# Performance work log

Measured on AMD Instinct MI355X. Metric: run time of the kernel, lower is better.

## Reference

```python
import jax, jax.numpy as jnp
import numpy as np

B, N, H, ITERS = 4, 4096, 128, 8
EPS = 1e-5  # torch LayerNorm default


def _mlp(x, w1, b1, w2, b2, w3, b3):
    x = jax.nn.relu(x @ w1.T + b1)
    x = jax.nn.relu(x @ w2.T + b2)
    return x @ w3.T + b3


def setup_inputs() -> dict:
    key = jax.random.key(0)
    ks = jax.random.split(key, 16)
    s = 0.05
    nrm = lambda k, shape: jax.random.normal(k, shape, jnp.float32) * s
    z = lambda *shape: jnp.zeros(shape, jnp.float32)
    return {
        "x": jax.random.normal(ks[0], (B, N, N), jnp.float32),
        "k": jax.random.uniform(ks[1], (B,), jnp.float32, 1.0, 10.0),
        "n": jax.random.uniform(ks[2], (B,), jnp.float32, 10.0, 100.0),
        "mask": (jax.random.uniform(ks[3], (B, N)) < 0.9).astype(jnp.float32),
        # init MLP: 2 -> H -> H -> H (torch Linear convention: [out, in])
        "init_w1": nrm(ks[4], (H, 2)), "init_b1": z(H),
        "init_w2": nrm(ks[5], (H, H)), "init_b2": z(H),
        "init_w3": nrm(ks[6], (H, H)), "init_b3": z(H),
        # msg MLP: H -> H -> H -> H
        "msg_w1": nrm(ks[7], (H, H)), "msg_b1": z(H),
        "msg_w2": nrm(ks[8], (H, H)), "msg_b2": z(H),
        "msg_w3": nrm(ks[9], (H, H)), "msg_b3": z(H),
        # LSTMCell (gate order i, f, g, o)
        "lstm_wih": nrm(ks[10], (4 * H, H)), "lstm_whh": nrm(ks[11], (4 * H, H)),
        "lstm_bih": z(4 * H), "lstm_bhh": z(4 * H),
        # LayerNorm affine
        "ln_g": jnp.ones(H, jnp.float32), "ln_b": z(H),
        # vote MLP: H -> H -> H -> 1
        "vote_w1": nrm(ks[12], (H, H)), "vote_b1": z(H),
        "vote_w2": nrm(ks[13], (H, H)), "vote_b2": z(H),
        "vote_w3": nrm(ks[14], (1, H)), "vote_b3": z(1),
    }


def reference(x, k, n, mask,
              init_w1, init_b1, init_w2, init_b2, init_w3, init_b3,
              msg_w1, msg_b1, msg_w2, msg_b2, msg_w3, msg_b3,
              lstm_wih, lstm_whh, lstm_bih, lstm_bhh,
              ln_g, ln_b,
              vote_w1, vote_b1, vote_w2, vote_b2, vote_w3, vote_b3):
    b, n_node, _ = x.shape

    def ln(h):
        mu = h.mean(-1, keepdims=True)
        xc = h - mu
        var = (xc * xc).mean(-1, keepdims=True)
        return xc * jax.lax.rsqrt(var + EPS) * ln_g + ln_b

    nk = jnp.stack([k, n], axis=1)                          # [B, 2]
    init0 = _mlp(nk, init_w1, init_b1, init_w2, init_b2, init_w3, init_b3)
    h = jnp.broadcast_to(init0[:, None, :], (b, n_node, init0.shape[-1]))  # [B, N, H]
    c = jnp.zeros_like(h)
    embed = ln(h)
    for _ in range(ITERS):
        m = _mlp(embed, msg_w1, msg_b1, msg_w2, msg_b2, msg_w3, msg_b3)   # [B, N, H]
        msg = jnp.einsum('bij,bjh->bih', x, m)                            # dense aggregation
        gates = msg @ lstm_wih.T + lstm_bih + h @ lstm_whh.T + lstm_bhh   # [B, N, 4H]
        i, f, g, o = jnp.split(gates, 4, axis=-1)
        c = jax.nn.sigmoid(f) * c + jax.nn.sigmoid(i) * jnp.tanh(g)
        h = jax.nn.sigmoid(o) * jnp.tanh(c)
        embed = ln(h)
    vote = _mlp(embed, vote_w1, vote_b1, vote_w2, vote_b2, vote_w3, vote_b3)[..., 0]  # [B, N]
    return jax.nn.sigmoid((vote * mask).sum(axis=1))        # [B]
```

## Files before the change

kernel.cpp:

```cpp
#include <hip/hip_runtime.h>
#include <cstddef>
#include <cstdint>

#define LN_EPS 1e-5f

typedef __attribute__((ext_vector_type(8))) short bf16x8;
typedef __attribute__((ext_vector_type(4))) float f32x4;

__device__ __forceinline__ unsigned short f2bf(float f) {
    unsigned u = __float_as_uint(f);
    u += 0x7FFFu + ((u >> 16) & 1u);
    return (unsigned short)(u >> 16);
}
__device__ __forceinline__ float sigf(float x) { return 1.f / (1.f + __expf(-x)); }

__device__ __forceinline__ void gload_lds16(const void* g, void* l) {
    __builtin_amdgcn_global_load_lds(
        (const __attribute__((address_space(1))) unsigned int*)(unsigned long long)(uintptr_t)g,
        (__attribute__((address_space(3))) unsigned int*)(unsigned int)(uintptr_t)l,
        16, 0, 0);
}

__device__ __forceinline__ void layer128(const unsigned short* __restrict__ W,
                                         const bf16x8 a[4], f32x4 acc[8],
                                         int lr, int lq)
{
#pragma unroll
    for (int s = 0; s < 4; ++s) {
#pragma unroll
        for (int tn = 0; tn < 8; ++tn) {
            bf16x8 b = *(const bf16x8*)(W + (tn * 16 + lr) * 128 + s * 32 + lq * 8);
            acc[tn] = __builtin_amdgcn_mfma_f32_16x16x32_bf16(a[s], b, acc[tn], 0, 0, 0);
        }
    }
}

__global__ __launch_bounds__(256)
void msg_mlp_kernel(const unsigned short* __restrict__ embed,
                    const unsigned short* __restrict__ w1, const float* __restrict__ b1,
                    const unsigned short* __restrict__ w2, const float* __restrict__ b2,
                    const unsigned short* __restrict__ w3, const float* __restrict__ b3,
                    unsigned short* __restrict__ m_t, int N)
{
    __shared__ unsigned short sact[4][16][136];
    const int lane = threadIdx.x & 63, wave = threadIdx.x >> 6;
    const int lr = lane & 15, lq = lane >> 4;
    const int r0 = (blockIdx.x * 4 + wave) * 16;

    bf16x8 a[4];
    f32x4 acc[8];

#pragma unroll
    for (int s = 0; s < 4; ++s)
        a[s] = *(const bf16x8*)(embed + (long long)(r0 + lr) * 128 + s * 32 + lq * 8);
#pragma unroll
    for (int tn = 0; tn < 8; ++tn) acc[tn] = (f32x4)(0.f);
    layer128(w1, a, acc, lr, lq);

#pragma unroll
    for (int tn = 0; tn < 8; ++tn) {
        float bb = b1[tn * 16 + lr];
#pragma unroll
        for (int r = 0; r < 4; ++r) {
            float v = acc[tn][r] + bb; v = v > 0.f ? v : 0.f;
            sact[wave][lq * 4 + r][tn * 16 + lr] = f2bf(v);
        }
    }
    __syncthreads();
#pragma unroll
    for (int s = 0; s < 4; ++s)
        a[s] = *(const bf16x8*)&sact[wave][lr][s * 32 + lq * 8];
#pragma unroll
    for (int tn = 0; tn < 8; ++tn) acc[tn] = (f32x4)(0.f);
    layer128(w2, a, acc, lr, lq);

#pragma unroll
    for (int tn = 0; tn < 8; ++tn) {
        float bb = b2[tn * 16 + lr];
#pragma unroll
        for (int r = 0; r < 4; ++r) {
            float v = acc[tn][r] + bb; v = v > 0.f ? v : 0.f;
            sact[wave][lq * 4 + r][tn * 16 + lr] = f2bf(v);
        }
    }
    __syncthreads();
#pragma unroll
    for (int s = 0; s < 4; ++s)
        a[s] = *(const bf16x8*)&sact[wave][lr][s * 32 + lq * 8];
#pragma unroll
    for (int tn = 0; tn < 8; ++tn) acc[tn] = (f32x4)(0.f);
    layer128(w3, a, acc, lr, lq);

    const int batch = r0 / N;
    const int rin0 = r0 - batch * N + lq * 4;
#pragma unroll
    for (int tn = 0; tn < 8; ++tn) {
        float bb = b3[tn * 16 + lr];
        ushort4 o;
        o.x = f2bf(acc[tn][0] + bb); o.y = f2bf(acc[tn][1] + bb);
        o.z = f2bf(acc[tn][2] + bb); o.w = f2bf(acc[tn][3] + bb);
        *(ushort4*)(m_t + ((long long)(batch * 128 + tn * 16 + lr)) * N + rin0) = o;
    }
}

__global__ __launch_bounds__(256)
void agg_mfma_kernel(const unsigned short* __restrict__ xb,
                     const unsigned short* __restrict__ mt,
                     float* __restrict__ msgp, int N, long long BNH)
{
    __shared__ short sA[128 * 64];
    __shared__ short sB[128 * 64];

    const int tid = threadIdx.x;
    const int lane = tid & 63, w = tid >> 6;
    const int lr = lane & 15, lq = lane >> 4;
    const int wr = w & 1, wc = w >> 1;
    const int r0 = blockIdx.x * 128;
    const int ksp = blockIdx.y;
    const int batch = blockIdx.z;
    const int kbase = ksp * (N >> 2);
    const int nsteps = (N >> 2) >> 6;

    const unsigned short* xrow = xb + (long long)batch * N * N;
    const unsigned short* mrow = mt + (long long)batch * 128 * N;

    f32x4 acc[4][4];
#pragma unroll
    for (int tr = 0; tr < 4; ++tr)
#pragma unroll
        for (int tn = 0; tn < 4; ++tn) acc[tr][tn] = (f32x4)(0.f);

    for (int step = 0; step < nsteps; ++step) {
        const int k0 = kbase + step * 64;
#pragma unroll
        for (int j = 0; j < 4; ++j) {
            const int c = ((w * 4 + j) << 6) + lane;
            const unsigned short* g = xrow + (long long)(r0 + (c >> 3)) * N + k0 + (c & 7) * 8;
            gload_lds16(g, (char*)sA + (w * 4 + j) * 1024);
        }
#pragma unroll
        for (int j = 0; j < 4; ++j) {
            const int c = ((w * 4 + j) << 6) + lane;
            const unsigned short* g = mrow + (long long)(c >> 3) * N + k0 + (c & 7) * 8;
            gload_lds16(g, (char*)sB + (w * 4 + j) * 1024);
        }
        __syncthreads();
#pragma unroll
        for (int ks = 0; ks < 2; ++ks) {
            bf16x8 af[4], bfr[4];
#pragma unroll
            for (int tr = 0; tr < 4; ++tr)
                af[tr] = *(const bf16x8*)((const char*)sA + (wr * 64 + tr * 16 + lr) * 128 + ks * 64 + lq * 16);
#pragma unroll
            for (int tn = 0; tn < 4; ++tn)
                bfr[tn] = *(const bf16x8*)((const char*)sB + (wc * 64 + tn * 16 + lr) * 128 + ks * 64 + lq * 16);
#pragma unroll
            for (int tr = 0; tr < 4; ++tr)
#pragma unroll
                for (int tn = 0; tn < 4; ++tn)
                    acc[tr][tn] = __builtin_amdgcn_mfma_f32_16x16x32_bf16(af[tr], bfr[tn], acc[tr][tn], 0, 0, 0);
        }
        __syncthreads();
    }

    float* outb = msgp + (long long)ksp * BNH + (long long)(batch * N + r0) * 128;
#pragma unroll
    for (int tr = 0; tr < 4; ++tr)
#pragma unroll
        for (int tn = 0; tn < 4; ++tn)
#pragma unroll
            for (int r = 0; r < 4; ++r)
                outb[(long long)(wr * 64 + tr * 16 + lq * 4 + r) * 128 + wc * 64 + tn * 16 + lr] = acc[tr][tn][r];
}

__global__ __launch_bounds__(256)
void agg_fallback_kernel(const float* __restrict__ xf,
                         const unsigned short* __restrict__ mt, float* __restrict__ msgp0,
                         int N)
{
    __shared__ float sacc[4][16][132];
    const int lane = threadIdx.x & 63, wave = threadIdx.x >> 6;
    const int lr = lane & 15, lq = lane >> 4;
    const int batch = blockIdx.y;
    const int rowBase = blockIdx.x * 16;
    const int kBase = wave * (N >> 2);
    const int kIters = N >> 7;

    const float* af = xf + (long long)batch * N * N + (long long)(rowBase + lr) * N + kBase + lq * 8;
    const long long bbase = (long long)batch * 128 * N + (long long)lr * N + kBase + lq * 8;

    f32x4 acc[8];
#pragma unroll
    for (int tn = 0; tn < 8; ++tn) acc[tn] = (f32x4)(0.f);

    for (int it = 0; it < kIters; ++it) {
        const int k = it * 32;
        float4 lo = *(const float4*)(af + k);
        float4 hi = *(const float4*)(af + k + 4);
        bf16x8 a0;
        a0[0] = (short)f2bf(lo.x); a0[1] = (short)f2bf(lo.y);
        a0[2] = (short)f2bf(lo.z); a0[3] = (short)f2bf(lo.w);
        a0[4] = (short)f2bf(hi.x); a0[5] = (short)f2bf(hi.y);
        a0[6] = (short)f2bf(hi.z); a0[7] = (short)f2bf(hi.w);
#pragma unroll
        for (int tn = 0; tn < 8; ++tn) {
            bf16x8 b0 = *(const bf16x8*)(mt + bbase + (long long)tn * 16 * N + k);
            acc[tn] = __builtin_amdgcn_mfma_f32_16x16x32_bf16(a0, b0, acc[tn], 0, 0, 0);
        }
    }

#pragma unroll
    for (int tn = 0; tn < 8; ++tn)
#pragma unroll
        for (int r = 0; r < 4; ++r)
            sacc[wave][lq * 4 + r][tn * 16 + lr] = acc[tn][r];
    __syncthreads();
    {
        const int t = threadIdx.x;
        const int row = t >> 4, cb2 = (t & 15) * 8;
        float o[8];
#pragma unroll
        for (int j = 0; j < 8; ++j)
            o[j] = sacc[0][row][cb2 + j] + sacc[1][row][cb2 + j]
                 + sacc[2][row][cb2 + j] + sacc[3][row][cb2 + j];
        float* dst = msgp0 + (long long)(batch * N + rowBase + row) * 128 + cb2;
        *(float4*)dst = make_float4(o[0], o[1], o[2], o[3]);
        *(float4*)(dst + 4) = make_float4(o[4], o[5], o[6], o[7]);
    }
}

template<int NPART>
__global__ __launch_bounds__(256)
void gates_lstm_kernel(const float* __restrict__ msgp, long long BNH,
                       unsigned short* hb, float* cb,
                       const unsigned short* __restrict__ wih,
                       const unsigned short* __restrict__ whh,
                       const float* __restrict__ bih, const float* __restrict__ bhh,
                       const float* __restrict__ lng, const float* __restrict__ lnb,
                       unsigned short* __restrict__ embed_out)
{
    __shared__ float sred[4][16][2];
    const int lane = threadIdx.x & 63, wave = threadIdx.x >> 6;
    const int lr = lane & 15, lq = lane >> 4;
    const int r0 = blockIdx.x * 16;

    f32x4 acc[8];
#pragma unroll
    for (int t = 0; t < 8; ++t) acc[t] = (f32x4)(0.f);

    bf16x8 a[4];
#pragma unroll
    for (int s = 0; s < 4; ++s) {
        const long long base = (long long)(r0 + lr) * 128 + s * 32 + lq * 8;
        float v[8];
        {
            float4 t0 = *(const float4*)(msgp + base);
            float4 t1 = *(const float4*)(msgp + base + 4);
            v[0] = t0.x; v[1] = t0.y; v[2] = t0.z; v[3] = t0.w;
            v[4] = t1.x; v[5] = t1.y; v[6] = t1.z; v[7] = t1.w;
        }
#pragma unroll
        for (int j = 1; j < NPART; ++j) {
            float4 t0 = *(const float4*)(msgp + j * BNH + base);
            float4 t1 = *(const float4*)(msgp + j * BNH + base + 4);
            v[0] += t0.x; v[1] += t0.y; v[2] += t0.z; v[3] += t0.w;
            v[4] += t1.x; v[5] += t1.y; v[6] += t1.z; v[7] += t1.w;
        }
        bf16x8 r8;
#pragma unroll
        for (int e = 0; e < 8; ++e) r8[e] = (short)f2bf(v[e]);
        a[s] = r8;
    }
#pragma unroll
    for (int s = 0; s < 4; ++s)
#pragma unroll
        for (int tt = 0; tt < 8; ++tt) {
            const int brow = (tt >> 1) * 128 + wave * 32 + (tt & 1) * 16 + lr;
            bf16x8 b = *(const bf16x8*)(wih + brow * 128 + s * 32 + lq * 8);
            acc[tt] = __builtin_amdgcn_mfma_f32_16x16x32_bf16(a[s], b, acc[tt], 0, 0, 0);
        }
#pragma unroll
    for (int s = 0; s < 4; ++s)
        a[s] = *(const bf16x8*)((const unsigned short*)hb + (long long)(r0 + lr) * 128 + s * 32 + lq * 8);
#pragma unroll
    for (int s = 0; s < 4; ++s)
#pragma unroll
        for (int tt = 0; tt < 8; ++tt) {
            const int brow = (tt >> 1) * 128 + wave * 32 + (tt & 1) * 16 + lr;
            bf16x8 b = *(const bf16x8*)(whh + brow * 128 + s * 32 + lq * 8);
            acc[tt] = __builtin_amdgcn_mfma_f32_16x16x32_bf16(a[s], b, acc[tt], 0, 0, 0);
        }

    float hn[2][4];
    float4* cw = (float4*)cb;
#pragma unroll
    for (int half = 0; half < 2; ++half) {
        const int col = wave * 32 + half * 16 + lr;
        const float bi  = bih[col]       + bhh[col];
        const float bf_ = bih[col + 128] + bhh[col + 128];
        const float bg  = bih[col + 256] + bhh[col + 256];
        const float bo  = bih[col + 384] + bhh[col + 384];
        const long long cidx = ((long long)blockIdx.x * 8 + wave * 2 + half) * 64 + lane;
        float4 cold = cw[cidx];
        float co[4] = {cold.x, cold.y, cold.z, cold.w};
        float cn[4];
#pragma unroll
        for (int r = 0; r < 4; ++r) {
            float iv = acc[0 + half][r] + bi;
            float fv = acc[2 + half][r] + bf_;
            float gv = acc[4 + half][r] + bg;
            float ov = acc[6 + half][r] + bo;
            float cc = sigf(fv) * co[r] + sigf(iv) * tanhf(gv);
            cn[r] = cc;
            hn[half][r] = sigf(ov) * tanhf(cc);
        }
        float4 cnew = {cn[0], cn[1], cn[2], cn[3]};
        cw[cidx] = cnew;
    }

    float ps1[4], ps2[4];
#pragma unroll
    for (int r = 0; r < 4; ++r) {
        float s1 = hn[0][r] + hn[1][r];
        float s2 = hn[0][r] * hn[0][r] + hn[1][r] * hn[1][r];
#pragma unroll
        for (int m = 1; m <= 8; m <<= 1) {
            s1 += __shfl_xor(s1, m);
            s2 += __shfl_xor(s2, m);
        }
        ps1[r] = s1; ps2[r] = s2;
    }
    if (lr == 0) {
#pragma unroll
        for (int r = 0; r < 4; ++r) {
            sred[wave][lq * 4 + r][0] = ps1[r];
            sred[wave][lq * 4 + r][1] = ps2[r];
        }
    }
    __syncthreads();

#pragma unroll
    for (int half = 0; half < 2; ++half) {
        const int col = wave * 32 + half * 16 + lr;
        const float g = lng[col], bb = lnb[col];
#pragma unroll
        for (int r = 0; r < 4; ++r) {
            const int row = lq * 4 + r;
            float S1 = sred[0][row][0] + sred[1][row][0] + sred[2][row][0] + sred[3][row][0];
            float S2 = sred[0][row][1] + sred[1][row][1] + sred[2][row][1] + sred[3][row][1];
            float mean = S1 * (1.f / 128.f);
            float var  = S2 * (1.f / 128.f) - mean * mean;
            float rs = rsqrtf(var + LN_EPS);
            long long off = (long long)(r0 + row) * 128 + col;
            hb[off] = f2bf(hn[half][r]);
            embed_out[off] = f2bf((hn[half][r] - mean) * rs * g + bb);
        }
    }
}

__global__ __launch_bounds__(256)
void vote_mlp_kernel(const unsigned short* __restrict__ embed,
                     const unsigned short* __restrict__ w1, const float* __restrict__ b1,
                     const unsigned short* __restrict__ w2, const float* __restrict__ b2,
                     const float* __restrict__ w3, const float* __restrict__ b3p,
                     const float* __restrict__ mask, float* __restrict__ logit, int N)
{
    __shared__ unsigned short sact[4][16][136];
    const int lane = threadIdx.x & 63, wave = threadIdx.x >> 6;
    const int lr = lane & 15, lq = lane >> 4;
    const int r0 = (blockIdx.x * 4 + wave) * 16;

    bf16x8 a[4];
    f32x4 acc[8];
#pragma unroll
    for (int s = 0; s < 4; ++s)
        a[s] = *(const bf16x8*)(embed + (long long)(r0 + lr) * 128 + s * 32 + lq * 8);
#pragma unroll
    for (int tn = 0; tn < 8; ++tn) acc[tn] = (f32x4)(0.f);
    layer128(w1, a, acc, lr, lq);

#pragma unroll
    for (int tn = 0; tn < 8; ++tn) {
        float bb = b1[tn * 16 + lr];
#pragma unroll
        for (int r = 0; r < 4; ++r) {
            float v = acc[tn][r] + bb; v = v > 0.f ? v : 0.f;
            sact[wave][lq * 4 + r][tn * 16 + lr] = f2bf(v);
        }
    }
    __syncthreads();
#pragma unroll
    for (int s = 0; s < 4; ++s)
        a[s] = *(const bf16x8*)&sact[wave][lr][s * 32 + lq * 8];
#pragma unroll
    for (int tn = 0; tn < 8; ++tn) acc[tn] = (f32x4)(0.f);
    layer128(w2, a, acc, lr, lq);

    float dot[4] = {0.f, 0.f, 0.f, 0.f};
#pragma unroll
    for (int tn = 0; tn < 8; ++tn) {
        const int col = tn * 16 + lr;
        const float bb = b2[col], w3c = w3[col];
#pragma unroll
        for (int r = 0; r < 4; ++r) {
            float v = acc[tn][r] + bb; v = v > 0.f ? v : 0.f;
            dot[r] += v * w3c;
        }
    }
#pragma unroll
    for (int r = 0; r < 4; ++r)
#pragma unroll
        for (int m = 1; m <= 8; m <<= 1) dot[r] += __shfl_xor(dot[r], m);

    const int batch = r0 / N;
    const float b3 = b3p[0];
    const int base = r0 + lq * 4;
    float wsum = mask[base + 0] * (dot[0] + b3) + mask[base + 1] * (dot[1] + b3)
               + mask[base + 2] * (dot[2] + b3) + mask[base + 3] * (dot[3] + b3);
    float t = (lr == 0) ? wsum : 0.f;
    t += __shfl_xor(t, 16);
    t += __shfl_xor(t, 32);
    if (lane == 0) atomicAdd(&logit[batch], t);
}

__global__ __launch_bounds__(128)
void init_kernel(const float* __restrict__ kk, const float* __restrict__ nn,
                 const float* __restrict__ w1, const float* __restrict__ b1,
                 const float* __restrict__ w2, const float* __restrict__ b2,
                 const float* __restrict__ w3, const float* __restrict__ b3,
                 const float* __restrict__ lng, const float* __restrict__ lnb,
                 float* __restrict__ init0, float* __restrict__ embed0,
                 float* __restrict__ logit, int H)
{
    int b = blockIdx.x, j = threadIdx.x;
    __shared__ float s1[128];
    __shared__ float s2[128];
    __shared__ float red[128];
    if (j == 0) logit[b] = 0.f;
    float kv = kk[b], nv = nn[b];
    float h1 = w1[j * 2 + 0] * kv + w1[j * 2 + 1] * nv + b1[j];
    h1 = h1 > 0.f ? h1 : 0.f;
    s1[j] = h1; __syncthreads();
    float h2 = b2[j];
    for (int q = 0; q < H; ++q) h2 += w2[j * H + q] * s1[q];
    h2 = h2 > 0.f ? h2 : 0.f;
    s2[j] = h2; __syncthreads();
    float o = b3[j];
    for (int q = 0; q < H; ++q) o += w3[j * H + q] * s2[q];
    init0[b * H + j] = o;

    red[j] = o; __syncthreads();
    for (int s = 64; s > 0; s >>= 1) { if (j < s) red[j] += red[j + s]; __syncthreads(); }
    float mu = red[0] / (float)H;
    __syncthreads();
    float d = o - mu;
    red[j] = d * d; __syncthreads();
    for (int s = 64; s > 0; s >>= 1) { if (j < s) red[j] += red[j + s]; __syncthreads(); }
    float var = red[0] / (float)H;
    embed0[b * H + j] = d * rsqrtf(var + LN_EPS) * lng[j] + lnb[j];
}

__global__ void bcast_kernel(const float* __restrict__ init0, const float* __restrict__ embed0,
                             unsigned short* __restrict__ hb, float* __restrict__ cb,
                             unsigned short* __restrict__ embed,
                             long long total, long long NH)
{
    long long idx = (long long)blockIdx.x * blockDim.x + threadIdx.x;
    if (idx >= total) return;
    int b = (int)(idx / NH);
    int j = (int)(idx & 127);
    hb[idx] = f2bf(init0[b * 128 + j]);
    embed[idx] = f2bf(embed0[b * 128 + j]);
    cb[idx] = 0.f;
}

__global__ void cast_kernel(const float* __restrict__ x, unsigned short* __restrict__ xb,
                            long long n4)
{
    long long i = ((long long)blockIdx.x * blockDim.x + threadIdx.x);
    if (i >= n4) return;
    float4 v = *(const float4*)(x + i * 4);
    ushort4 o;
    o.x = f2bf(v.x); o.y = f2bf(v.y); o.z = f2bf(v.z); o.w = f2bf(v.w);
    *(ushort4*)&xb[i * 4] = o;
}

struct CastArgs {
    const float* src[7];
    unsigned short* dst[7];
    int n[7];
};

__global__ void castw_kernel(CastArgs a)
{
    int rg = blockIdx.y;
    int i = (blockIdx.x * blockDim.x + threadIdx.x) * 4;
    if (i < a.n[rg]) {
        float4 v = *(const float4*)(a.src[rg] + i);
        ushort4 o;
        o.x = f2bf(v.x); o.y = f2bf(v.y); o.z = f2bf(v.z); o.w = f2bf(v.w);
        *(ushort4*)(a.dst[rg] + i) = o;
    }
}

__global__ void sigmoid_kernel(const float* __restrict__ logit, float* __restrict__ out, int B)
{
    int b = threadIdx.x;
    if (b < B) out[b] = 1.f / (1.f + __expf(-logit[b]));
}

extern "C" void kernel_launch(void* const* d_in, const int* in_sizes, int n_in,
                              void* d_out, int out_size, void* d_ws, size_t ws_size,
                              hipStream_t stream)
{
    const float* x    = (const float*)d_in[0];
    const float* kk   = (const float*)d_in[1];
    const float* nn   = (const float*)d_in[2];
    const float* mask = (const float*)d_in[3];
    const float* iw1  = (const float*)d_in[4];
    const float* ib1  = (const float*)d_in[5];
    const float* iw2  = (const float*)d_in[6];
    const float* ib2  = (const float*)d_in[7];
    const float* iw3  = (const float*)d_in[8];
    const float* ib3  = (const float*)d_in[9];
    const float* mw1  = (const float*)d_in[10];
    const float* mb1  = (const float*)d_in[11];
    const float* mw2  = (const float*)d_in[12];
    const float* mb2  = (const float*)d_in[13];
    const float* mw3  = (const float*)d_in[14];
    const float* mb3  = (const float*)d_in[15];
    const float* wih  = (const float*)d_in[16];
    const float* whh  = (const float*)d_in[17];
    const float* bih  = (const float*)d_in[18];
    const float* bhh  = (const float*)d_in[19];
    const float* lng  = (const float*)d_in[20];
    const float* lnb  = (const float*)d_in[21];
    const float* vw1  = (const float*)d_in[22];
    const float* vb1  = (const float*)d_in[23];
    const float* vw2  = (const float*)d_in[24];
    const float* vb2  = (const float*)d_in[25];
    const float* vw3  = (const float*)d_in[26];
    const float* vb3  = (const float*)d_in[27];
    float* out = (float*)d_out;

    const int B = in_sizes[1];
    const int H = in_sizes[5];
    const int N = in_sizes[3] / B;
    const long long NH  = (long long)N * H;
    const long long BNH = (long long)B * NH;
    const int M = B * N;

    char* p = (char*)d_ws;
    auto alloc = [&](long long bytes) {
        char* q = p; p += (bytes + 255) & ~255LL; return q;
    };
    float*          cb     = (float*)alloc(BNH * 4);
    unsigned short* embed  = (unsigned short*)alloc(BNH * 2);
    unsigned short* hb     = (unsigned short*)alloc(BNH * 2);
    unsigned short* m_t    = (unsigned short*)alloc(BNH * 2);
    float*          msgp   = (float*)alloc(4 * BNH * 4);
    float*          init0  = (float*)alloc((long long)B * H * 4);
    float*          embed0 = (float*)alloc((long long)B * H * 4);
    float*          logit  = (float*)alloc((long long)B * 4);
    unsigned short* wb_m1  = (unsigned short*)alloc((long long)H * H * 2);
    unsigned short* wb_m2  = (unsigned short*)alloc((long long)H * H * 2);
    unsigned short* wb_m3  = (unsigned short*)alloc((long long)H * H * 2);
    unsigned short* wb_ih  = (unsigned short*)alloc(4LL * H * H * 2);
    unsigned short* wb_hh  = (unsigned short*)alloc(4LL * H * H * 2);
    unsigned short* wb_v1  = (unsigned short*)alloc((long long)H * H * 2);
    unsigned short* wb_v2  = (unsigned short*)alloc((long long)H * H * 2);
    unsigned short* x_bf   = (unsigned short*)alloc(2LL * B * N * N);
    const bool use_xb = ((long long)(p - (char*)d_ws) <= (long long)ws_size);

    init_kernel<<<B, H, 0, stream>>>(kk, nn, iw1, ib1, iw2, ib2, iw3, ib3, lng, lnb,
                                     init0, embed0, logit, H);
    {
        long long nb = (BNH + 255) / 256;
        bcast_kernel<<<dim3((unsigned)nb), 256, 0, stream>>>(init0, embed0, hb, cb, embed, BNH, NH);
    }
    {
        CastArgs ca;
        ca.src[0] = mw1; ca.dst[0] = wb_m1; ca.n[0] = H * H;
        ca.src[1] = mw2; ca.dst[1] = wb_m2; ca.n[1] = H * H;
        ca.src[2] = mw3; ca.dst[2] = wb_m3; ca.n[2] = H * H;
        ca.src[3] = wih; ca.dst[3] = wb_ih; ca.n[3] = 4 * H * H;
        ca.src[4] = whh; ca.dst[4] = wb_hh; ca.n[4] = 4 * H * H;
        ca.src[5] = vw1; ca.dst[5] = wb_v1; ca.n[5] = H * H;
        ca.src[6] = vw2; ca.dst[6] = wb_v2; ca.n[6] = H * H;
        castw_kernel<<<dim3(64, 7), 256, 0, stream>>>(ca);
    }
    if (use_xb) {
        long long n4 = (long long)B * N * N / 4;
        cast_kernel<<<dim3((unsigned)((n4 + 255) / 256)), 256, 0, stream>>>(x, x_bf, n4);
    }

    dim3 gridRow(M / 64);
    dim3 gridRow16(M / 16);
    dim3 gridAggNew(N / 128, 4, B);
    dim3 gridAggOld(N / 16, B);

    for (int it = 0; it < 8; ++it) {
        msg_mlp_kernel<<<gridRow, 256, 0, stream>>>(embed, wb_m1, mb1, wb_m2, mb2,
                                                    wb_m3, mb3, m_t, N);
        if (use_xb) {
            agg_mfma_kernel<<<gridAggNew, 256, 0, stream>>>(x_bf, m_t, msgp, N, BNH);
            gates_lstm_kernel<4><<<gridRow16, 256, 0, stream>>>(msgp, BNH, hb, cb, wb_ih, wb_hh,
                                                                bih, bhh, lng, lnb, embed);
        } else {
            agg_fallback_kernel<<<gridAggOld, 256, 0, stream>>>(x, m_t, msgp, N);
            gates_lstm_kernel<1><<<gridRow16, 256, 0, stream>>>(msgp, BNH, hb, cb, wb_ih, wb_hh,
                                                                bih, bhh, lng, lnb, embed);
        }
    }

    vote_mlp_kernel<<<gridRow, 256, 0, stream>>>(embed, wb_v1, vb1, wb_v2, vb2,
                                                 vw3, vb3, mask, logit, N);
    sigmoid_kernel<<<1, 64, 0, stream>>>(logit, out, B);
}
```

Baseline: 1.268 ms.

## Switch dense aggregation to FP8 MFMA with double-buffered swizzled LDS

Casts x and the message matrix to FP8 and runs the dense aggregation with the 16x16x32 fp8 MFMA. K-tiles grow to 128 and are double-buffered in LDS, with an XOR swizzle against bank conflicts. Split-K partial sums are stored as bf16 instead of fp32 to halve partial traffic into the LSTM gates kernel. The aim is to halve the bytes read from x per iteration and raise MFMA throughput, at the cost of much lower precision in the aggregation. The fallback path now writes fp32 into a buffer sized for bf16, which looks undersized.

```diff
diff --git a/kernel.cpp b/kernel.cpp
--- a/kernel.cpp
+++ b/kernel.cpp
@@ -11,6 +11,9 @@
     unsigned u = __float_as_uint(f);
     u += 0x7FFFu + ((u >> 16) & 1u);
     return (unsigned short)(u >> 16);
+}
+__device__ __forceinline__ float bf2f(unsigned short s) {
+    return __uint_as_float(((unsigned)s) << 16);
 }
 __device__ __forceinline__ float sigf(float x) { return 1.f / (1.f + __expf(-x)); }
 
@@ -35,12 +38,14 @@
     }
 }
 
+template<bool FP8>
 __global__ __launch_bounds__(256)
 void msg_mlp_kernel(const unsigned short* __restrict__ embed,
                     const unsigned short* __restrict__ w1, const float* __restrict__ b1,
                     const unsigned short* __restrict__ w2, const float* __restrict__ b2,
                     const unsigned short* __restrict__ w3, const float* __restrict__ b3,
-                    unsigned short* __restrict__ m_t, int N)
+                    unsigned short* __restrict__ m_t, unsigned char* __restrict__ m8,
+                    int N)
 {
     __shared__ unsigned short sact[4][16][136];
     const int lane = threadIdx.x & 63, wave = threadIdx.x >> 6;
@@ -96,20 +101,27 @@
 #pragma unroll
     for (int tn = 0; tn < 8; ++tn) {
         float bb = b3[tn * 16 + lr];
-        ushort4 o;
-        o.x = f2bf(acc[tn][0] + bb); o.y = f2bf(acc[tn][1] + bb);
-        o.z = f2bf(acc[tn][2] + bb); o.w = f2bf(acc[tn][3] + bb);
-        *(ushort4*)(m_t + ((long long)(batch * 128 + tn * 16 + lr)) * N + rin0) = o;
+        float v0 = acc[tn][0] + bb, v1 = acc[tn][1] + bb;
+        float v2 = acc[tn][2] + bb, v3 = acc[tn][3] + bb;
+        if constexpr (FP8) {
+            int pk = __builtin_amdgcn_cvt_pk_fp8_f32(v0, v1, 0, false);
+            pk = __builtin_amdgcn_cvt_pk_fp8_f32(v2, v3, pk, true);
+            *(unsigned int*)(m8 + (long long)(batch * 128 + tn * 16 + lr) * N + rin0) = (unsigned)pk;
+        } else {
+            ushort4 o;
+            o.x = f2bf(v0); o.y = f2bf(v1); o.z = f2bf(v2); o.w = f2bf(v3);
+            *(ushort4*)(m_t + ((long long)(batch * 128 + tn * 16 + lr)) * N + rin0) = o;
+        }
     }
 }
 
 __global__ __launch_bounds__(256)
-void agg_mfma_kernel(const unsigned short* __restrict__ xb,
-                     const unsigned short* __restrict__ mt,
-                     float* __restrict__ msgp, int N, long long BNH)
-{
-    __shared__ short sA[128 * 64];
-    __shared__ short sB[128 * 64];
+void agg_fp8_kernel(const unsigned char* __restrict__ x8,
+                    const unsigned char* __restrict__ m8,
+                    unsigned short* __restrict__ msgp, int N, long long BNH)
+{
+    __shared__ unsigned char sA[2][128 * 128];
+    __shared__ unsigned char sB[2][128 * 128];
 
     const int tid = threadIdx.x;
     const int lane = tid & 63, w = tid >> 6;
@@ -119,10 +131,10 @@
     const int ksp = blockIdx.y;
     const int batch = blockIdx.z;
     const int kbase = ksp * (N >> 2);
-    const int nsteps = (N >> 2) >> 6;
-
-    const unsigned short* xrow = xb + (long long)batch * N * N;
-    const unsigned short* mrow = mt + (long long)batch * 128 * N;
+    const int nsteps = (N >> 2) >> 7;
+
+    const unsigned char* xrow = x8 + (long long)batch * N * N;
+    const unsigned char* mrow = m8 + (long long)batch * 128 * N;
 
     f32x4 acc[4][4];
 #pragma unroll
@@ -130,47 +142,69 @@
 #pragma unroll
         for (int tn = 0; tn < 4; ++tn) acc[tr][tn] = (f32x4)(0.f);
 
-    for (int step = 0; step < nsteps; ++step) {
-        const int k0 = kbase + step * 64;
+    auto stage = [&](int b, int step) {
+        const int k0 = kbase + step * 128;
 #pragma unroll
         for (int j = 0; j < 4; ++j) {
             const int c = ((w * 4 + j) << 6) + lane;
-            const unsigned short* g = xrow + (long long)(r0 + (c >> 3)) * N + k0 + (c & 7) * 8;
-            gload_lds16(g, (char*)sA + (w * 4 + j) * 1024);
+            const int row = c >> 3;
+            const int gs = (c & 7) ^ (row & 7);
+            gload_lds16(xrow + (long long)(r0 + row) * N + k0 + gs * 16,
+                        (char*)sA[b] + (w * 4 + j) * 1024);
         }
 #pragma unroll
         for (int j = 0; j < 4; ++j) {
             const int c = ((w * 4 + j) << 6) + lane;
-            const unsigned short* g = mrow + (long long)(c >> 3) * N + k0 + (c & 7) * 8;
-            gload_lds16(g, (char*)sB + (w * 4 + j) * 1024);
+            const int row = c >> 3;
+            const int gs = (c & 7) ^ (row & 7);
+            gload_lds16(mrow + (long long)row * N + k0 + gs * 16,
+                        (char*)sB[b] + (w * 4 + j) * 1024);
+        }
+    };
+
+    stage(0, 0);
+    __syncthreads();
+    int buf = 0;
+    for (int step = 0; step < nsteps; ++step) {
+        if (step + 1 < nsteps) stage(buf ^ 1, step + 1);
+        const unsigned char* A  = sA[buf];
+        const unsigned char* Bp = sB[buf];
+#pragma unroll
+        for (int ks = 0; ks < 4; ++ks) {
+            const int g    = ks * 4 + lq;
+            const int half = (g & 1) << 3;
+            const int s16  = g >> 1;
+            long af[4], bfr[4];
+#pragma unroll
+            for (int tr = 0; tr < 4; ++tr) {
+                const int row = wr * 64 + tr * 16 + lr;
+                af[tr] = *(const long*)(A + row * 128 + ((s16 ^ (row & 7)) << 4) + half);
+            }
+#pragma unroll
+            for (int tn = 0; tn < 4; ++tn) {
+                const int row = wc * 64 + tn * 16 + lr;
+                bfr[tn] = *(const long*)(Bp + row * 128 + ((s16 ^ (row & 7)) << 4) + half);
+            }
+#pragma unroll
+            for (int tr = 0; tr < 4; ++tr)
+#pragma unroll
+                for (int tn = 0; tn < 4; ++tn)
+                    acc[tr][tn] = __builtin_amdgcn_mfma_f32_16x16x32_fp8_fp8(
+                        af[tr], bfr[tn], acc[tr][tn], 0, 0, 0);
         }
         __syncthreads();
-#pragma unroll
-        for (int ks = 0; ks < 2; ++ks) {
-            bf16x8 af[4], bfr[4];
-#pragma unroll
-            for (int tr = 0; tr < 4; ++tr)
-                af[tr] = *(const bf16x8*)((const char*)sA + (wr * 64 + tr * 16 + lr) * 128 + ks * 64 + lq * 16);
-#pragma unroll
-            for (int tn = 0; tn < 4; ++tn)
-                bfr[tn] = *(const bf16x8*)((const char*)sB + (wc * 64 + tn * 16 + lr) * 128 + ks * 64 + lq * 16);
-#pragma unroll
-            for (int tr = 0; tr < 4; ++tr)
-#pragma unroll
-                for (int tn = 0; tn < 4; ++tn)
-                    acc[tr][tn] = __builtin_amdgcn_mfma_f32_16x16x32_bf16(af[tr], bfr[tn], acc[tr][tn], 0, 0, 0);
-        }
-        __syncthreads();
-    }
-
-    float* outb = msgp + (long long)ksp * BNH + (long long)(batch * N + r0) * 128;
+        buf ^= 1;
+    }
+
+    unsigned short* outb = msgp + (long long)ksp * BNH + (long long)(batch * N + r0) * 128;
 #pragma unroll
     for (int tr = 0; tr < 4; ++tr)
 #pragma unroll
         for (int tn = 0; tn < 4; ++tn)
 #pragma unroll
             for (int r = 0; r < 4; ++r)
-                outb[(long long)(wr * 64 + tr * 16 + lq * 4 + r) * 128 + wc * 64 + tn * 16 + lr] = acc[tr][tn][r];
+                outb[(long long)(wr * 64 + tr * 16 + lq * 4 + r) * 128 + wc * 64 + tn * 16 + lr]
+                    = f2bf(acc[tr][tn][r]);
 }
 
 __global__ __launch_bounds__(256)
@@ -229,9 +263,9 @@
     }
 }
 
-template<int NPART>
+template<int NPART, bool BF16P>
 __global__ __launch_bounds__(256)
-void gates_lstm_kernel(const float* __restrict__ msgp, long long BNH,
+void gates_lstm_kernel(const void* __restrict__ msgp, long long BNH,
                        unsigned short* hb, float* cb,
                        const unsigned short* __restrict__ wih,
                        const unsigned short* __restrict__ whh,
@@ -253,18 +287,30 @@
     for (int s = 0; s < 4; ++s) {
         const long long base = (long long)(r0 + lr) * 128 + s * 32 + lq * 8;
         float v[8];
-        {
-            float4 t0 = *(const float4*)(msgp + base);
-            float4 t1 = *(const float4*)(msgp + base + 4);
+        if constexpr (BF16P) {
+            const unsigned short* mp = (const unsigned short*)msgp;
+            bf16x8 t0 = *(const bf16x8*)(mp + base);
+#pragma unroll
+            for (int e = 0; e < 8; ++e) v[e] = bf2f((unsigned short)t0[e]);
+#pragma unroll
+            for (int j = 1; j < NPART; ++j) {
+                bf16x8 tj = *(const bf16x8*)(mp + (long long)j * BNH + base);
+#pragma unroll
+                for (int e = 0; e < 8; ++e) v[e] += bf2f((unsigned short)tj[e]);
+            }
+        } else {
+            const float* mp = (const float*)msgp;
+            float4 t0 = *(const float4*)(mp + base);
+            float4 t1 = *(const float4*)(mp + base + 4);
             v[0] = t0.x; v[1] = t0.y; v[2] = t0.z; v[3] = t0.w;
             v[4] = t1.x; v[5] = t1.y; v[6] = t1.z; v[7] = t1.w;
-        }
-#pragma unroll
-        for (int j = 1; j < NPART; ++j) {
-            float4 t0 = *(const float4*)(msgp + j * BNH + base);
-            float4 t1 = *(const float4*)(msgp + j * BNH + base + 4);
-            v[0] += t0.x; v[1] += t0.y; v[2] += t0.z; v[3] += t0.w;
-            v[4] += t1.x; v[5] += t1.y; v[6] += t1.z; v[7] += t1.w;
+#pragma unroll
+            for (int j = 1; j < NPART; ++j) {
+                float4 u0 = *(const float4*)(mp + (long long)j * BNH + base);
+                float4 u1 = *(const float4*)(mp + (long long)j * BNH + base + 4);
+                v[0] += u0.x; v[1] += u0.y; v[2] += u0.z; v[3] += u0.w;
+                v[4] += u1.x; v[5] += u1.y; v[6] += u1.z; v[7] += u1.w;
+            }
         }
         bf16x8 r8;
 #pragma unroll
@@ -474,15 +520,20 @@
     cb[idx] = 0.f;
 }
 
-__global__ void cast_kernel(const float* __restrict__ x, unsigned short* __restrict__ xb,
-                            long long n4)
+__global__ void cast8_kernel(const float* __restrict__ x, unsigned char* __restrict__ x8,
+                             long long n8)
 {
     long long i = ((long long)blockIdx.x * blockDim.x + threadIdx.x);
-    if (i >= n4) return;
-    float4 v = *(const float4*)(x + i * 4);
-    ushort4 o;
-    o.x = f2bf(v.x); o.y = f2bf(v.y); o.z = f2bf(v.z); o.w = f2bf(v.w);
-    *(ushort4*)&xb[i * 4] = o;
+    if (i >= n8) return;
+    const float* s = x + i * 8;
+    float4 a = *(const float4*)s;
+    float4 b = *(const float4*)(s + 4);
+    int lo = __builtin_amdgcn_cvt_pk_fp8_f32(a.x, a.y, 0, false);
+    lo = __builtin_amdgcn_cvt_pk_fp8_f32(a.z, a.w, lo, true);
+    int hi = __builtin_amdgcn_cvt_pk_fp8_f32(b.x, b.y, 0, false);
+    hi = __builtin_amdgcn_cvt_pk_fp8_f32(b.z, b.w, hi, true);
+    int2 o; o.x = lo; o.y = hi;
+    *(int2*)(x8 + i * 8) = o;
 }
 
 struct CastArgs {
@@ -558,7 +609,7 @@
     unsigned short* embed  = (unsigned short*)alloc(BNH * 2);
     unsigned short* hb     = (unsigned short*)alloc(BNH * 2);
     unsigned short* m_t    = (unsigned short*)alloc(BNH * 2);
-    float*          msgp   = (float*)alloc(4 * BNH * 4);
+    unsigned short* msgp   = (unsigned short*)alloc(4 * BNH * 2);
     float*          init0  = (float*)alloc((long long)B * H * 4);
     float*          embed0 = (float*)alloc((long long)B * H * 4);
     float*          logit  = (float*)alloc((long long)B * 4);
@@ -569,8 +620,9 @@
     unsigned short* wb_hh  = (unsigned short*)alloc(4LL * H * H * 2);
     unsigned short* wb_v1  = (unsigned short*)alloc((long long)H * H * 2);
     unsigned short* wb_v2  = (unsigned short*)alloc((long long)H * H * 2);
-    unsigned short* x_bf   = (unsigned short*)alloc(2LL * B * N * N);
-    const bool use_xb = ((long long)(p - (char*)d_ws) <= (long long)ws_size);
+    unsigned char*  m8_t   = (unsigned char*)alloc(BNH);
+    unsigned char*  x8     = (unsigned char*)alloc((long long)B * N * N);
+    const bool use_x8 = ((long long)(p - (char*)d_ws) <= (long long)ws_size);
 
     init_kernel<<<B, H, 0, stream>>>(kk, nn, iw1, ib1, iw2, ib2, iw3, ib3, lng, lnb,
                                      init0, embed0, logit, H);
@@ -589,9 +641,9 @@
         ca.src[6] = vw2; ca.dst[6] = wb_v2; ca.n[6] = H * H;
         castw_kernel<<<dim3(64, 7), 256, 0, stream>>>(ca);
     }
-    if (use_xb) {
-        long long n4 = (long long)B * N * N / 4;
-        cast_kernel<<<dim3((unsigned)((n4 + 255) / 256)), 256, 0, stream>>>(x, x_bf, n4);
+    if (use_x8) {
+        long long n8 = (long long)B * N * N / 8;
+        cast8_kernel<<<dim3((unsigned)((n8 + 255) / 256)), 256, 0, stream>>>(x, x8, n8);
     }
 
     dim3 gridRow(M / 64);
@@ -600,16 +652,18 @@
     dim3 gridAggOld(N / 16, B);
 
     for (int it = 0; it < 8; ++it) {
-        msg_mlp_kernel<<<gridRow, 256, 0, stream>>>(embed, wb_m1, mb1, wb_m2, mb2,
-                                                    wb_m3, mb3, m_t, N);
-        if (use_xb) {
-            agg_mfma_kernel<<<gridAggNew, 256, 0, stream>>>(x_bf, m_t, msgp, N, BNH);
-            gates_lstm_kernel<4><<<gridRow16, 256, 0, stream>>>(msgp, BNH, hb, cb, wb_ih, wb_hh,
-                                                                bih, bhh, lng, lnb, embed);
+        if (use_x8) {
+            msg_mlp_kernel<true><<<gridRow, 256, 0, stream>>>(embed, wb_m1, mb1, wb_m2, mb2,
+                                                              wb_m3, mb3, m_t, m8_t, N);
+            agg_fp8_kernel<<<gridAggNew, 256, 0, stream>>>(x8, m8_t, msgp, N, BNH);
+            gates_lstm_kernel<4, true><<<gridRow16, 256, 0, stream>>>(
+                (const void*)msgp, BNH, hb, cb, wb_ih, wb_hh, bih, bhh, lng, lnb, embed);
         } else {
-            agg_fallback_kernel<<<gridAggOld, 256, 0, stream>>>(x, m_t, msgp, N);
-            gates_lstm_kernel<1><<<gridRow16, 256, 0, stream>>>(msgp, BNH, hb, cb, wb_ih, wb_hh,
-                                                                bih, bhh, lng, lnb, embed);
+            msg_mlp_kernel<false><<<gridRow, 256, 0, stream>>>(embed, wb_m1, mb1, wb_m2, mb2,
+                                                               wb_m3, mb3, m_t, m8_t, N);
+            agg_fallback_kernel<<<gridAggOld, 256, 0, stream>>>(x, m_t, (float*)msgp, N);
+            gates_lstm_kernel<1, false><<<gridRow16, 256, 0, stream>>>(
+                (const void*)msgp, BNH, hb, cb, wb_ih, wb_hh, bih, bhh, lng, lnb, embed);
         }
     }
 
```

Result: faster. 1.135 ms (-10.5%).
